# Kernel tuning notes

Hardware: AMD Instinct MI355X
Metric: run time of the kernel (lower is better)

## Reference

```python
import jax, jax.numpy as jnp
import numpy as np

B, S, V, H, L, NH, DH, F = 1, 512, 30522, 768, 12, 12, 64, 3072
N, E, GH, NC = 50000, 800000, 128, 3


def setup_inputs() -> dict:
    key = jax.random.key(0)
    ks = iter(jax.random.split(key, 48))
    def nrm(shape, s=0.02):
        return jax.random.normal(next(ks), shape, jnp.float32) * s
    inp = {
        "input_ids": jax.random.randint(next(ks), (B, S), 0, V, dtype=jnp.int32),
        "attention_mask": jnp.ones((B, S), jnp.int32),
        "token_type_ids": jnp.zeros((B, S), jnp.int32),
        "premise_edge_index": jax.random.randint(next(ks), (2, E), 0, N, dtype=jnp.int32),
        "hypothesis_edge_index": jax.random.randint(next(ks), (2, E), 0, N, dtype=jnp.int32),
        "premise_node_features": nrm((N, H), 1.0),
        "hypothesis_node_features": nrm((N, H), 1.0),
        "word_emb": nrm((V, H)), "pos_emb": nrm((S, H)), "type_emb": nrm((2, H)),
        "emb_ln_s": jnp.ones((H,)), "emb_ln_b": jnp.zeros((H,)),
        "Wq": nrm((L, H, H)), "bq": jnp.zeros((L, H)),
        "Wk": nrm((L, H, H)), "bk": jnp.zeros((L, H)),
        "Wv": nrm((L, H, H)), "bv": jnp.zeros((L, H)),
        "Wo": nrm((L, H, H)), "bo": jnp.zeros((L, H)),
        "ln1_s": jnp.ones((L, H)), "ln1_b": jnp.zeros((L, H)),
        "W1": nrm((L, H, F)), "b1": jnp.zeros((L, F)),
        "W2": nrm((L, F, H)), "b2": jnp.zeros((L, H)),
        "ln2_s": jnp.ones((L, H)), "ln2_b": jnp.zeros((L, H)),
        "gcn_W1": nrm((H, GH), 0.05), "gcn_b1": jnp.zeros((GH,)),
        "gcn_W2": nrm((GH, GH), 0.05), "gcn_b2": jnp.zeros((GH,)),
        "comb_W": nrm((2 * (H + GH), H)), "comb_b": jnp.zeros((H,)),
        "cls_W": nrm((H, NC)), "cls_b": jnp.zeros((NC,)),
    }
    return inp


def _ln(x, s, b, eps=1e-12):
    m = jnp.mean(x, -1, keepdims=True)
    v = jnp.mean(jnp.square(x - m), -1, keepdims=True)
    return (x - m) * jax.lax.rsqrt(v + eps) * s + b


def _gcn(x, edge_index, W1, b1, W2, b2):
    # PyG GCNConv: add self-loops, symmetric D^-1/2 A D^-1/2 normalization,
    # linear transform first, then scatter-add messages at destination.
    n = x.shape[0]
    loops = jnp.arange(n, dtype=edge_index.dtype)
    src = jnp.concatenate([edge_index[0], loops])
    dst = jnp.concatenate([edge_index[1], loops])
    deg = jax.ops.segment_sum(jnp.ones(src.shape[0], jnp.float32), dst, num_segments=n)
    dinv = jnp.where(deg > 0, jax.lax.rsqrt(jnp.maximum(deg, 1e-12)), 0.0)
    norm = (dinv[src] * dinv[dst])[:, None]
    def conv(h, W, b):
        hw = h @ W
        return jax.ops.segment_sum(hw[src] * norm, dst, num_segments=n) + b
    h = jax.nn.relu(conv(x, W1, b1))
    h = conv(h, W2, b2)
    # global_mean_pool with batch=None -> single graph mean, shape [1, GH]
    return jnp.mean(h, axis=0, keepdims=True)


def _bert(input_ids, attention_mask, token_type_ids, word_emb, pos_emb, type_emb, emb_ln_s, emb_ln_b, layer_params):
    s = input_ids.shape[1]
    h = word_emb[input_ids] + pos_emb[None, :s] + type_emb[token_type_ids]
    h = _ln(h, emb_ln_s, emb_ln_b)
    bias = (1.0 - attention_mask.astype(jnp.float32))[:, None, None, :] * -1e4
    def step(h, p):
        wq, bq, wk, bk, wv, bv, wo, bo, l1s, l1b, w1, b1_, w2, b2_, l2s, l2b = p
        b_, s_, _ = h.shape
        q = (h @ wq + bq).reshape(b_, s_, NH, DH)
        k = (h @ wk + bk).reshape(b_, s_, NH, DH)
        v = (h @ wv + bv).reshape(b_, s_, NH, DH)
        scores = jnp.einsum('bqhd,bkhd->bhqk', q, k) / np.float32(np.sqrt(DH)) + bias
        ctx = jnp.einsum('bhqk,bkhd->bqhd', jax.nn.softmax(scores, -1), v).reshape(b_, s_, H)
        h1 = _ln(h + ctx @ wo + bo, l1s, l1b)
        f = jax.nn.gelu(h1 @ w1 + b1_, approximate=False) @ w2 + b2_
        return _ln(h1 + f, l2s, l2b), None
    h, _ = jax.lax.scan(step, h, layer_params)
    return h[:, 0, :]  # CLS pooling, [B, H]


def reference(input_ids, attention_mask, token_type_ids, premise_edge_index, premise_node_features, hypothesis_edge_index, hypothesis_node_features, word_emb, pos_emb, type_emb, emb_ln_s, emb_ln_b, Wq, bq, Wk, bk, Wv, bv, Wo, bo, ln1_s, ln1_b, W1, b1, W2, b2, ln2_s, ln2_b, gcn_W1, gcn_b1, gcn_W2, gcn_b2, comb_W, comb_b, cls_W, cls_b):
    lp = (Wq, bq, Wk, bk, Wv, bv, Wo, bo, ln1_s, ln1_b, W1, b1, W2, b2, ln2_s, ln2_b)
    cls = _bert(input_ids, attention_mask, token_type_ids, word_emb, pos_emb, type_emb, emb_ln_s, emb_ln_b, lp)
    gp = _gcn(premise_node_features, premise_edge_index, gcn_W1, gcn_b1, gcn_W2, gcn_b2)
    gh = _gcn(hypothesis_node_features, hypothesis_edge_index, gcn_W1, gcn_b1, gcn_W2, gcn_b2)
    cp = jnp.concatenate([cls, gp], -1)
    ch = jnp.concatenate([cls, gh], -1)
    fc = jnp.concatenate([cp, ch], -1)  # [1, 2*(H+GH)]
    feat = jax.nn.relu(fc @ comb_W + comb_b)  # dropout is identity at eval
    return feat @ cls_W + cls_b
```

## Files before the change

### kernel.cpp

```cpp
#include <hip/hip_runtime.h>
#include <math.h>

constexpr int kS = 512, kH = 768, kNH = 12, kDH = 64, kF = 3072, kL = 12;
constexpr int kN = 50000, kE = 800000, kGH = 128;

#define CDIV(a,b) (((a)+(b)-1)/(b))

struct Ptr3 { const float* p[3]; };

typedef __attribute__((ext_vector_type(8))) short bf16x8;
typedef __attribute__((ext_vector_type(4))) float f32x4;

__device__ __forceinline__ unsigned short bf16_rne(float f) {
    unsigned int u = __float_as_uint(f);
    u += 0x7fffu + ((u >> 16) & 1u);
    return (unsigned short)(u >> 16);
}
__device__ __forceinline__ float bf16_f32(unsigned short h) {
    return __uint_as_float(((unsigned int)h) << 16);
}
__device__ __forceinline__ void split2(float f, short& hi, short& lo) {
    unsigned short h = bf16_rne(f);
    hi = (short)h;
    lo = (short)bf16_rne(f - bf16_f32(h));
}

constexpr int LDR = 72;

__global__ void fill_kernel(float* p, float v, long n) {
    long i = blockIdx.x * (long)blockDim.x + threadIdx.x;
    if (i < n) p[i] = v;
}

__global__ void gcn_zero_kernel(int* icnt, float* wsum, float* svec) {
    int i = blockIdx.x * 256 + threadIdx.x;
    if (i < kN) { icnt[i] = 0; wsum[i] = 0.f; }
    if (i < kGH) svec[i] = 0.f;
}

__global__ void embed_ln_kernel(const int* ids, const int* tt, const int* mask,
                                const float* we, const float* pe, const float* te,
                                const float* g, const float* b, float* out,
                                short* oh, short* ol, float* mb) {
    int s = blockIdx.x;
    int tid = threadIdx.x;
    __shared__ float red[256];
    if (tid == 0) mb[s] = (1.f - (float)mask[s]) * -1e4f;
    int id = ids[s], t = tt[s];
    float vals[3]; float sum = 0.f;
    #pragma unroll
    for (int r = 0; r < 3; r++) {
        int j = tid + r * 256;
        float x = we[(long)id * kH + j] + pe[(long)s * kH + j] + te[(long)t * kH + j];
        vals[r] = x; sum += x;
    }
    red[tid] = sum; __syncthreads();
    for (int off = 128; off > 0; off >>= 1) { if (tid < off) red[tid] += red[tid + off]; __syncthreads(); }
    float mean = red[0] / kH; __syncthreads();
    float vs = 0.f;
    #pragma unroll
    for (int r = 0; r < 3; r++) { float d = vals[r] - mean; vs += d * d; }
    red[tid] = vs; __syncthreads();
    for (int off = 128; off > 0; off >>= 1) { if (tid < off) red[tid] += red[tid + off]; __syncthreads(); }
    float rstd = rsqrtf(red[0] / kH + 1e-12f);
    #pragma unroll
    for (int r = 0; r < 3; r++) {
        int j = tid + r * 256;
        float o = (vals[r] - mean) * rstd * g[j] + b[j];
        out[(long)s * kH + j] = o;
        short hi, lo; split2(o, hi, lo);
        oh[(long)s * kH + j] = hi; ol[(long)s * kH + j] = lo;
    }
}

__global__ void wtrans_all_kernel(const float* __restrict__ W, short* __restrict__ Th,
                                  short* __restrict__ Tl, int K, int N, long ostride) {
    int z = blockIdx.z;
    const float* Wm = W + (long)z * K * N;
    long moff = (long)z * ostride;
    __shared__ short th[32][33], tl[32][33];
    int n0 = blockIdx.x * 32, k0 = blockIdx.y * 32;
    int c = threadIdx.x & 31, r = threadIdx.x >> 5;
    #pragma unroll
    for (int p = 0; p < 4; p++) {
        int rr = p * 8 + r;
        float f = Wm[(long)(k0 + rr) * N + n0 + c];
        short hi, lo; split2(f, hi, lo);
        th[rr][c] = hi; tl[rr][c] = lo;
    }
    __syncthreads();
    #pragma unroll
    for (int p = 0; p < 4; p++) {
        int rr = p * 8 + r;
        Th[moff + (long)(n0 + rr) * K + k0 + c] = th[c][rr];
        Tl[moff + (long)(n0 + rr) * K + k0 + c] = tl[c][rr];
    }
}

__global__ void vtrans_kernel(const short* __restrict__ vh, const short* __restrict__ vl,
                              short* __restrict__ vth, short* __restrict__ vtl) {
    __shared__ short th[32][33], tl[32][33];
    int s0 = blockIdx.x * 32;
    int h = blockIdx.y >> 1, d0 = (blockIdx.y & 1) * 32;
    int c = threadIdx.x & 31, r = threadIdx.x >> 5;
    #pragma unroll
    for (int p = 0; p < 4; p++) {
        int rr = p * 8 + r;
        th[rr][c] = vh[(long)(s0 + rr) * kH + h * kDH + d0 + c];
        tl[rr][c] = vl[(long)(s0 + rr) * kH + h * kDH + d0 + c];
    }
    __syncthreads();
    #pragma unroll
    for (int p = 0; p < 4; p++) {
        int rr = p * 8 + r;
        vth[((long)h * kDH + d0 + rr) * kS + s0 + c] = th[c][rr];
        vtl[((long)h * kDH + d0 + rr) * kS + s0 + c] = tl[c][rr];
    }
}

__global__ __launch_bounds__(256, 4) void gemm64_pre(
    const short* __restrict__ Ah, const short* __restrict__ Al,
    const short* __restrict__ Bth, const short* __restrict__ Btl, long wstride,
    float* __restrict__ part, int M, int Nn, int K, int S)
{
    __shared__ short As[64 * LDR], Bs[128 * LDR];
    int w = blockIdx.z / S, s = blockIdx.z % S;
    const short* Bh_ = Bth + (long)w * wstride;
    const short* Bl_ = Btl + (long)w * wstride;
    int Kc = K / S, kbeg = s * Kc;
    int m0 = blockIdx.y * 64, n0 = blockIdx.x * 128;
    int tid = threadIdx.x;
    int ar = tid >> 2, aq = (tid & 3) * 8;
    const short* Agh = Ah + (long)(m0 + ar) * K + kbeg + aq;
    const short* Agl = Al + (long)(m0 + ar) * K + kbeg + aq;
    int aofs = ar * LDR + aq;
    int br = tid >> 1, bq = (tid & 1) * 16;
    const short* Bgh = Bh_ + (long)(n0 + br) * K + kbeg + bq;
    const short* Bgl = Bl_ + (long)(n0 + br) * K + kbeg + bq;
    int bofs = br * LDR + bq;
    int wid = tid >> 6, lane = tid & 63;
    int wm = (wid >> 1) * 32, wn = (wid & 1) * 64;
    int fr = lane & 15, ko = (lane >> 4) * 8;
    f32x4 acc[2][4];
    #pragma unroll
    for (int i = 0; i < 2; i++)
        #pragma unroll
        for (int j = 0; j < 4; j++) acc[i][j] = (f32x4){0.f, 0.f, 0.f, 0.f};
    int nst = Kc / 32;
    bf16x8 pa0 = *(const bf16x8*)(Agh);
    bf16x8 pa1 = *(const bf16x8*)(Agl);
    bf16x8 pb0 = *(const bf16x8*)(Bgh);
    bf16x8 pb1 = *(const bf16x8*)(Bgh + 8);
    bf16x8 pb2 = *(const bf16x8*)(Bgl);
    bf16x8 pb3 = *(const bf16x8*)(Bgl + 8);
    for (int st = 0; st < nst; ++st) {
        *(bf16x8*)&As[aofs]      = pa0;
        *(bf16x8*)&As[aofs + 32] = pa1;
        *(bf16x8*)&Bs[bofs]      = pb0;
        *(bf16x8*)&Bs[bofs + 8]  = pb1;
        *(bf16x8*)&Bs[bofs + 32] = pb2;
        *(bf16x8*)&Bs[bofs + 40] = pb3;
        if (st + 1 < nst) {
            int go = (st + 1) * 32;
            pa0 = *(const bf16x8*)(Agh + go);
            pa1 = *(const bf16x8*)(Agl + go);
            pb0 = *(const bf16x8*)(Bgh + go);
            pb1 = *(const bf16x8*)(Bgh + go + 8);
            pb2 = *(const bf16x8*)(Bgl + go);
            pb3 = *(const bf16x8*)(Bgl + go + 8);
        }
        __syncthreads();
        bf16x8 bh[4], bl[4];
        #pragma unroll
        for (int j = 0; j < 4; j++) {
            int c = (wn + j * 16 + fr) * LDR + ko;
            bh[j] = *(const bf16x8*)&Bs[c];
            bl[j] = *(const bf16x8*)&Bs[c + 32];
        }
        #pragma unroll
        for (int i = 0; i < 2; i++) {
            int r = (wm + i * 16 + fr) * LDR + ko;
            bf16x8 ah = *(const bf16x8*)&As[r];
            bf16x8 al = *(const bf16x8*)&As[r + 32];
            #pragma unroll
            for (int j = 0; j < 4; j++) {
                acc[i][j] = __builtin_amdgcn_mfma_f32_16x16x32_bf16(ah, bh[j], acc[i][j], 0, 0, 0);
                acc[i][j] = __builtin_amdgcn_mfma_f32_16x16x32_bf16(ah, bl[j], acc[i][j], 0, 0, 0);
                acc[i][j] = __builtin_amdgcn_mfma_f32_16x16x32_bf16(al, bh[j], acc[i][j], 0, 0, 0);
            }
        }
        __syncthreads();
    }
    long MN = (long)M * Nn;
    float* Pp = part + (long)(w * S + s) * MN;
    int cr = (lane >> 4) * 4;
    #pragma unroll
    for (int i = 0; i < 2; i++) {
        #pragma unroll
        for (int r = 0; r < 4; r++) {
            int gm = m0 + wm + i * 16 + cr + r;
            float* rowp = &Pp[(long)gm * Nn + n0 + wn + fr];
            #pragma unroll
            for (int j = 0; j < 4; j++) rowp[j * 16] = acc[i][j][r];
        }
    }
}

__global__ __launch_bounds__(256, 4) void gemm64_gcn(
    const float* __restrict__ A,
    const short* __restrict__ Bth, const short* __restrict__ Btl,
    float* __restrict__ part, int M, int Nn, int K, int S)
{
    __shared__ short As[64 * LDR], Bs[128 * LDR];
    int s = blockIdx.z;
    int Kc = K / S, kbeg = s * Kc;
    int m0 = blockIdx.y * 64, n0 = blockIdx.x * 128;
    int tid = threadIdx.x;
    int ar = tid >> 2, aqf = (tid & 3) * 8;
    int gmA = m0 + ar; if (gmA > M - 1) gmA = M - 1;
    const float* Agf = A + (long)gmA * K + kbeg + aqf;
    int aofs = ar * LDR + aqf;
    int br = tid >> 1, bq = (tid & 1) * 16;
    const short* Bgh = Bth + (long)(n0 + br) * K + kbeg + bq;
    const short* Bgl = Btl + (long)(n0 + br) * K + kbeg + bq;
    int bofs = br * LDR + bq;
    int wid = tid >> 6, lane = tid & 63;
    int wm = (wid >> 1) * 32, wn = (wid & 1) * 64;
    int fr = lane & 15, ko = (lane >> 4) * 8;
    f32x4 acc[2][4];
    #pragma unroll
    for (int i = 0; i < 2; i++)
        #pragma unroll
        for (int j = 0; j < 4; j++) acc[i][j] = (f32x4){0.f, 0.f, 0.f, 0.f};
    int nst = Kc / 32;
    float4 pf0 = *(const float4*)(Agf);
    float4 pf1 = *(const float4*)(Agf + 4);
    bf16x8 pb0 = *(const bf16x8*)(Bgh);
    bf16x8 pb1 = *(const bf16x8*)(Bgh + 8);
    bf16x8 pb2 = *(const bf16x8*)(Bgl);
    bf16x8 pb3 = *(const bf16x8*)(Bgl + 8);
    for (int st = 0; st < nst; ++st) {
        short h0, l0, h1, l1, h2, l2, h3, l3, h4, l4, h5, l5, h6, l6, h7, l7;
        split2(pf0.x, h0, l0); split2(pf0.y, h1, l1); split2(pf0.z, h2, l2); split2(pf0.w, h3, l3);
        split2(pf1.x, h4, l4); split2(pf1.y, h5, l5); split2(pf1.z, h6, l6); split2(pf1.w, h7, l7);
        *(short4*)&As[aofs]      = make_short4(h0, h1, h2, h3);
        *(short4*)&As[aofs + 4]  = make_short4(h4, h5, h6, h7);
        *(short4*)&As[aofs + 32] = make_short4(l0, l1, l2, l3);
        *(short4*)&As[aofs + 36] = make_short4(l4, l5, l6, l7);
        *(bf16x8*)&Bs[bofs]      = pb0;
        *(bf16x8*)&Bs[bofs + 8]  = pb1;
        *(bf16x8*)&Bs[bofs + 32] = pb2;
        *(bf16x8*)&Bs[bofs + 40] = pb3;
        if (st + 1 < nst) {
            int go = (st + 1) * 32;
            pf0 = *(const float4*)(Agf + go);
            pf1 = *(const float4*)(Agf + go + 4);
            pb0 = *(const bf16x8*)(Bgh + go);
            pb1 = *(const bf16x8*)(Bgh + go + 8);
            pb2 = *(const bf16x8*)(Bgl + go);
            pb3 = *(const bf16x8*)(Bgl + go + 8);
        }
        __syncthreads();
        bf16x8 bh[4], bl[4];
        #pragma unroll
        for (int j = 0; j < 4; j++) {
            int c = (wn + j * 16 + fr) * LDR + ko;
            bh[j] = *(const bf16x8*)&Bs[c];
            bl[j] = *(const bf16x8*)&Bs[c + 32];
        }
        #pragma unroll
        for (int i = 0; i < 2; i++) {
            int r = (wm + i * 16 + fr) * LDR + ko;
            bf16x8 ah = *(const bf16x8*)&As[r];
            bf16x8 al = *(const bf16x8*)&As[r + 32];
            #pragma unroll
            for (int j = 0; j < 4; j++) {
                acc[i][j] = __builtin_amdgcn_mfma_f32_16x16x32_bf16(ah, bh[j], acc[i][j], 0, 0, 0);
                acc[i][j] = __builtin_amdgcn_mfma_f32_16x16x32_bf16(ah, bl[j], acc[i][j], 0, 0, 0);
                acc[i][j] = __builtin_amdgcn_mfma_f32_16x16x32_bf16(al, bh[j], acc[i][j], 0, 0, 0);
            }
        }
        __syncthreads();
    }
    long MN = (long)M * Nn;
    float* Pp = part + (long)s * MN;
    int cr = (lane >> 4) * 4;
    #pragma unroll
    for (int i = 0; i < 2; i++) {
        #pragma unroll
        for (int r = 0; r < 4; r++) {
            int gm = m0 + wm + i * 16 + cr + r;
            if (gm >= M) continue;
            float* rowp = &Pp[(long)gm * Nn + n0 + wn + fr];
            #pragma unroll
            for (int j = 0; j < 4; j++) rowp[j * 16] = acc[i][j][r];
        }
    }
}

__global__ __launch_bounds__(128) void flash_attn_kernel(
    const short* __restrict__ qh, const short* __restrict__ ql,
    const short* __restrict__ kh, const short* __restrict__ kl,
    const short* __restrict__ vth, const short* __restrict__ vtl,
    const float* __restrict__ mb,
    short* __restrict__ ctxh, short* __restrict__ ctxl)
{
    __shared__ short Qs[2 * 64 * LDR];
    __shared__ short Ks[128 * LDR];
    __shared__ short Ps[4 * 64 * 40];
    int h = blockIdx.y;
    int q0 = blockIdx.x * 64;
    int tid = threadIdx.x;
    int wid = tid >> 6, lane = tid & 63;
    int wm = wid * 32;
    int fr = lane & 15, ko = (lane >> 4) * 8;
    int cr4 = (lane >> 4) * 4;
    {
        int row = tid >> 1, dseg = tid & 1;
        const short* gh_ = qh + (long)(q0 + row) * kH + h * kDH + dseg * 32;
        const short* gl_ = ql + (long)(q0 + row) * kH + h * kDH + dseg * 32;
        short* dst = &Qs[(dseg * 64 + row) * LDR];
        #pragma unroll
        for (int c = 0; c < 4; c++) {
            *(bf16x8*)&dst[c * 8]      = *(const bf16x8*)(gh_ + c * 8);
            *(bf16x8*)&dst[32 + c * 8] = *(const bf16x8*)(gl_ + c * 8);
        }
    }
    float mrun[2][4], lrun[2][4];
    f32x4 accO[2][4];
    #pragma unroll
    for (int i = 0; i < 2; i++)
        #pragma unroll
        for (int r = 0; r < 4; r++) { mrun[i][r] = -1e30f; lrun[i][r] = 0.f; }
    #pragma unroll
    for (int i = 0; i < 2; i++)
        #pragma unroll
        for (int j = 0; j < 4; j++) accO[i][j] = (f32x4){0.f, 0.f, 0.f, 0.f};

    for (int t = 0; t < 4; ++t) {
        int k0t = t * 128;
        f32x4 accS[2][8];
        #pragma unroll
        for (int i = 0; i < 2; i++)
            #pragma unroll
            for (int j = 0; j < 8; j++) accS[i][j] = (f32x4){0.f, 0.f, 0.f, 0.f};
        for (int st = 0; st < 2; ++st) {
            __syncthreads();
            {
                int row = tid;
                const short* gh_ = kh + (long)(k0t + row) * kH + h * kDH + st * 32;
                const short* gl_ = kl + (long)(k0t + row) * kH + h * kDH + st * 32;
                short* dst = &Ks[row * LDR];
                #pragma unroll
                for (int c = 0; c < 4; c++) {
                    *(bf16x8*)&dst[c * 8]      = *(const bf16x8*)(gh_ + c * 8);
                    *(bf16x8*)&dst[32 + c * 8] = *(const bf16x8*)(gl_ + c * 8);
                }
            }
            __syncthreads();
            bf16x8 bh[8], bl[8];
            #pragma unroll
            for (int j = 0; j < 8; j++) {
                int c = (j * 16 + fr) * LDR + ko;
                bh[j] = *(const bf16x8*)&Ks[c];
                bl[j] = *(const bf16x8*)&Ks[c + 32];
            }
            #pragma unroll
            for (int i = 0; i < 2; i++) {
                int r = (st * 64 + wm + i * 16 + fr) * LDR + ko;
                bf16x8 ah = *(const bf16x8*)&Qs[r];
                bf16x8 al = *(const bf16x8*)&Qs[r + 32];
                #pragma unroll
                for (int j = 0; j < 8; j++) {
                    accS[i][j] = __builtin_amdgcn_mfma_f32_16x16x32_bf16(ah, bh[j], accS[i][j], 0, 0, 0);
                    accS[i][j] = __builtin_amdgcn_mfma_f32_16x16x32_bf16(ah, bl[j], accS[i][j], 0, 0, 0);
                    accS[i][j] = __builtin_amdgcn_mfma_f32_16x16x32_bf16(al, bh[j], accS[i][j], 0, 0, 0);
                }
            }
        }
        float mbv[8];
        #pragma unroll
        for (int j = 0; j < 8; j++) mbv[j] = mb[k0t + j * 16 + fr];
        #pragma unroll
        for (int i = 0; i < 2; i++) {
            #pragma unroll
            for (int r = 0; r < 4; r++) {
                float mt = -1e30f;
                #pragma unroll
                for (int j = 0; j < 8; j++) {
                    float sv = accS[i][j][r] * 0.125f + mbv[j];
                    accS[i][j][r] = sv;
                    mt = fmaxf(mt, sv);
                }
                #pragma unroll
                for (int mmask = 1; mmask < 16; mmask <<= 1)
                    mt = fmaxf(mt, __shfl_xor(mt, mmask, 64));
                float mn = fmaxf(mrun[i][r], mt);
                float sc = __expf(mrun[i][r] - mn);
                mrun[i][r] = mn;
                lrun[i][r] *= sc;
                #pragma unroll
                for (int jo = 0; jo < 4; jo++) {
                    accO[i][jo][r] *= sc;
                }
                float lt = 0.f;
                #pragma unroll
                for (int j = 0; j < 8; j++) {
                    float p = __expf(accS[i][j][r] - mn);
                    accS[i][j][r] = p;
                    lt += p;
                }
                #pragma unroll
                for (int mmask = 1; mmask < 16; mmask <<= 1)
                    lt += __shfl_xor(lt, mmask, 64);
                lrun[i][r] += lt;
            }
        }
        #pragma unroll
        for (int i = 0; i < 2; i++)
            #pragma unroll
            for (int j = 0; j < 8; j++)
                #pragma unroll
                for (int r = 0; r < 4; r++) {
                    int rowp = wm + i * 16 + cr4 + r;
                    Ps[(j >> 1) * 2560 + rowp * 40 + (j & 1) * 16 + fr] =
                        (short)bf16_rne(accS[i][j][r]);
                }
        for (int st2 = 0; st2 < 4; ++st2) {
            __syncthreads();
            {
                int row = tid >> 1, half = tid & 1;
                const short* gh_ = vth + ((long)h * kDH + row) * kS + k0t + st2 * 32 + half * 16;
                const short* gl_ = vtl + ((long)h * kDH + row) * kS + k0t + st2 * 32 + half * 16;
                short* dst = &Ks[row * LDR + half * 16];
                *(bf16x8*)&dst[0]  = *(const bf16x8*)(gh_);
                *(bf16x8*)&dst[8]  = *(const bf16x8*)(gh_ + 8);
                *(bf16x8*)&dst[32] = *(const bf16x8*)(gl_);
                *(bf16x8*)&dst[40] = *(const bf16x8*)(gl_ + 8);
            }
            __syncthreads();
            bf16x8 vh_[4], vl_[4];
            #pragma unroll
            for (int j = 0; j < 4; j++) {
                int c = (j * 16 + fr) * LDR + ko;
                vh_[j] = *(const bf16x8*)&Ks[c];
                vl_[j] = *(const bf16x8*)&Ks[c + 32];
            }
            #pragma unroll
            for (int i = 0; i < 2; i++) {
                bf16x8 pa = *(const bf16x8*)&Ps[st2 * 2560 + (wm + i * 16 + fr) * 40 + ko];
                #pragma unroll
                for (int j = 0; j < 4; j++) {
                    accO[i][j] = __builtin_amdgcn_mfma_f32_16x16x32_bf16(pa, vh_[j], accO[i][j], 0, 0, 0);
                    accO[i][j] = __builtin_amdgcn_mfma_f32_16x16x32_bf16(pa, vl_[j], accO[i][j], 0, 0, 0);
                }
            }
        }
        __syncthreads();
        #pragma unroll
        for (int i = 0; i < 2; i++)
            #pragma unroll
            for (int j = 0; j < 8; j++)
                #pragma unroll
                for (int r = 0; r < 4; r++) {
                    int rowp = wm + i * 16 + cr4 + r;
                    float p = accS[i][j][r];
                    unsigned short ph = bf16_rne(p);
                    Ps[(j >> 1) * 2560 + rowp * 40 + (j & 1) * 16 + fr] =
                        (short)bf16_rne(p - bf16_f32(ph));
                }
        for (int st2 = 0; st2 < 4; ++st2) {
            __syncthreads();
            {
                int row = tid >> 1, half = tid & 1;
                const short* gh_ = vth + ((long)h * kDH + row) * kS + k0t + st2 * 32 + half * 16;
                short* dst = &Ks[row * LDR + half * 16];
                *(bf16x8*)&dst[0] = *(const bf16x8*)(gh_);
                *(bf16x8*)&dst[8] = *(const bf16x8*)(gh_ + 8);
            }
            __syncthreads();
            bf16x8 vh_[4];
            #pragma unroll
            for (int j = 0; j < 4; j++)
                vh_[j] = *(const bf16x8*)&Ks[(j * 16 + fr) * LDR + ko];
            #pragma unroll
            for (int i = 0; i < 2; i++) {
                bf16x8 pa = *(const bf16x8*)&Ps[st2 * 2560 + (wm + i * 16 + fr) * 40 + ko];
                #pragma unroll
                for (int j = 0; j < 4; j++)
                    accO[i][j] = __builtin_amdgcn_mfma_f32_16x16x32_bf16(pa, vh_[j], accO[i][j], 0, 0, 0);
            }
        }
        __syncthreads();
    }
    #pragma unroll
    for (int i = 0; i < 2; i++) {
        #pragma unroll
        for (int r = 0; r < 4; r++) {
            float inv = 1.f / lrun[i][r];
            int q = q0 + wm + i * 16 + cr4 + r;
            #pragma unroll
            for (int j = 0; j < 4; j++) {
                float o = accO[i][j][r] * inv;
                int col = h * kDH + j * 16 + fr;
                short hi, lo; split2(o, hi, lo);
                ctxh[(long)q * kH + col] = hi;
                ctxl[(long)q * kH + col] = lo;
            }
        }
    }
}

__global__ void splitk_epi_qkv_kernel(const float* __restrict__ part, Ptr3 bias,
                                      short* __restrict__ qh, short* __restrict__ ql,
                                      short* __restrict__ kh, short* __restrict__ kl,
                                      short* __restrict__ vh, short* __restrict__ vl,
                                      int S) {
    const long MN = (long)kS * kH;
    int w = blockIdx.y;
    long i = ((long)blockIdx.x * blockDim.x + threadIdx.x) * 4;
    if (i >= MN) return;
    const float* P = part + (long)w * S * MN + i;
    float4 a = *(const float4*)P;
    for (int s2 = 1; s2 < S; ++s2) {
        float4 b2 = *(const float4*)(P + (long)s2 * MN);
        a.x += b2.x; a.y += b2.y; a.z += b2.z; a.w += b2.w;
    }
    const float* bw = bias.p[w];
    int n = (int)(i % kH);
    a.x += bw[n]; a.y += bw[n + 1]; a.z += bw[n + 2]; a.w += bw[n + 3];
    short* oh = (w == 0) ? qh : (w == 1) ? kh : vh;
    short* ol = (w == 0) ? ql : (w == 1) ? kl : vl;
    short h0, l0, h1, l1, h2, l2, h3, l3;
    split2(a.x, h0, l0); split2(a.y, h1, l1); split2(a.z, h2, l2); split2(a.w, h3, l3);
    *(short4*)&oh[i] = make_short4(h0, h1, h2, h3);
    *(short4*)&ol[i] = make_short4(l0, l1, l2, l3);
}

__global__ void splitk_epi_sh_kernel(const float* __restrict__ part, const float* __restrict__ bias,
                                     short* __restrict__ oh, short* __restrict__ ol,
                                     long MN, int Nn, int S, int act) {
    long i = ((long)blockIdx.x * blockDim.x + threadIdx.x) * 4;
    if (i >= MN) return;
    const float* P = part + i;
    float4 a = *(const float4*)P;
    for (int s2 = 1; s2 < S; ++s2) {
        float4 b2 = *(const float4*)(P + (long)s2 * MN);
        a.x += b2.x; a.y += b2.y; a.z += b2.z; a.w += b2.w;
    }
    if (bias) {
        int n = (int)(i % Nn);
        a.x += bias[n]; a.y += bias[n + 1]; a.z += bias[n + 2]; a.w += bias[n + 3];
    }
    if (act == 1) {
        a.x = 0.5f * a.x * (1.f + erff(a.x * 0.70710678118654752f));
        a.y = 0.5f * a.y * (1.f + erff(a.y * 0.70710678118654752f));
        a.z = 0.5f * a.z * (1.f + erff(a.z * 0.70710678118654752f));
        a.w = 0.5f * a.w * (1.f + erff(a.w * 0.70710678118654752f));
    }
    short h0, l0, h1, l1, h2, l2, h3, l3;
    split2(a.x, h0, l0); split2(a.y, h1, l1); split2(a.z, h2, l2); split2(a.w, h3, l3);
    *(short4*)&oh[i] = make_short4(h0, h1, h2, h3);
    *(short4*)&ol[i] = make_short4(l0, l1, l2, l3);
}

__global__ void splitk_epi_ln2_kernel(const float* __restrict__ part, const float* __restrict__ bias,
                                      const float* __restrict__ res, const float* __restrict__ g,
                                      const float* __restrict__ b, float* __restrict__ out,
                                      short* __restrict__ oh, short* __restrict__ ol, int S) {
    int row = blockIdx.x; int tid = threadIdx.x;
    __shared__ float red[256];
    const long MN = (long)kS * kH;
    float vals[3]; float sum = 0.f;
    #pragma unroll
    for (int r = 0; r < 3; r++) {
        int j = tid + r * 256;
        const float* P = part + (long)row * kH + j;
        float x = res[(long)row * kH + j] + bias[j];
        for (int s2 = 0; s2 < S; ++s2) x += P[(long)s2 * MN];
        vals[r] = x; sum += x;
    }
    red[tid] = sum; __syncthreads();
    for (int off = 128; off > 0; off >>= 1) { if (tid < off) red[tid] += red[tid + off]; __syncthreads(); }
    float mean = red[0] / kH; __syncthreads();
    float vs = 0.f;
    #pragma unroll
    for (int r = 0; r < 3; r++) { float d = vals[r] - mean; vs += d * d; }
    red[tid] = vs; __syncthreads();
    for (int off = 128; off > 0; off >>= 1) { if (tid < off) red[tid] += red[tid + off]; __syncthreads(); }
    float rstd = rsqrtf(red[0] / kH + 1e-12f);
    #pragma unroll
    for (int r = 0; r < 3; r++) {
        int j = tid + r * 256;
        float o = (vals[r] - mean) * rstd * g[j] + b[j];
        out[(long)row * kH + j] = o;
        short hi, lo; split2(o, hi, lo);
        oh[(long)row * kH + j] = hi; ol[(long)row * kH + j] = lo;
    }
}

__global__ void cnt_kernel(const int* __restrict__ dst, int* __restrict__ cnt, int E) {
    int e = blockIdx.x * blockDim.x + threadIdx.x;
    if (e < E) atomicAdd(&cnt[dst[e]], 1);
}

__global__ void scan1_kernel(const int* __restrict__ cnt, int* __restrict__ offs,
                             int* __restrict__ bsum, int n) {
    __shared__ int sh[256];
    int i = blockIdx.x * 256 + threadIdx.x;
    int v = (i < n) ? cnt[i] : 0;
    sh[threadIdx.x] = v; __syncthreads();
    for (int off = 1; off < 256; off <<= 1) {
        int t = (threadIdx.x >= off) ? sh[threadIdx.x - off] : 0;
        __syncthreads();
        sh[threadIdx.x] += t;
        __syncthreads();
    }
    if (i < n) offs[i] = sh[threadIdx.x] - v;
    if (threadIdx.x == 255) bsum[blockIdx.x] = sh[255];
}

__global__ void scan2_kernel(int* bsum, int nb, int* offs, int n) {
    if (threadIdx.x == 0) {
        int run = 0;
        for (int b = 0; b < nb; b++) { int t = bsum[b]; bsum[b] = run; run += t; }
        offs[n] = run;
    }
}

__global__ void scan3_kernel(const int* __restrict__ cnt, int* __restrict__ offs,
                             const int* __restrict__ bsum, int* __restrict__ cur,
                             float* __restrict__ dinv, int n) {
    int i = blockIdx.x * 256 + threadIdx.x;
    if (i >= n) return;
    int o = offs[i] + bsum[blockIdx.x];
    offs[i] = o; cur[i] = o;
    dinv[i] = rsqrtf((float)(cnt[i] + 1));
}

__global__ void csrfill_edgew_kernel(const int* __restrict__ src, const int* __restrict__ dst,
                                     int* __restrict__ cur, int* __restrict__ csr,
                                     const float* __restrict__ dinv, float* __restrict__ wsum,
                                     int E) {
    int e = blockIdx.x * blockDim.x + threadIdx.x;
    if (e < E) {
        int s2 = src[e], d = dst[e];
        int slot = atomicAdd(&cur[d], 1);
        csr[slot] = s2;
        atomicAdd(&wsum[s2], dinv[s2] * dinv[d]);
    }
}

__global__ __launch_bounds__(256) void spmm_gather_kernel(const int* __restrict__ offs,
                                                          const int* __restrict__ csr,
                                                          const float* __restrict__ dinv,
                                                          const float* __restrict__ hw,
                                                          const float* __restrict__ b1,
                                                          float* __restrict__ hout, int n) {
    int d = blockIdx.x * 2 + (threadIdx.x >> 7);
    int j = threadIdx.x & 127;
    if (d >= n) return;
    int beg = offs[d], end = offs[d + 1];
    float a0 = 0.f, a1 = 0.f, a2 = 0.f, a3 = 0.f;
    float a4 = 0.f, a5 = 0.f, a6 = 0.f, a7 = 0.f;
    int p = beg;
    for (; p + 8 <= end; p += 8) {
        int s0 = csr[p], s1 = csr[p + 1], s2 = csr[p + 2], s3 = csr[p + 3];
        int s4 = csr[p + 4], s5 = csr[p + 5], s6 = csr[p + 6], s7 = csr[p + 7];
        a0 += dinv[s0] * hw[(long)s0 * kGH + j];
        a1 += dinv[s1] * hw[(long)s1 * kGH + j];
        a2 += dinv[s2] * hw[(long)s2 * kGH + j];
        a3 += dinv[s3] * hw[(long)s3 * kGH + j];
        a4 += dinv[s4] * hw[(long)s4 * kGH + j];
        a5 += dinv[s5] * hw[(long)s5 * kGH + j];
        a6 += dinv[s6] * hw[(long)s6 * kGH + j];
        a7 += dinv[s7] * hw[(long)s7 * kGH + j];
    }
    for (; p < end; ++p) {
        int s8 = csr[p];
        a0 += dinv[s8] * hw[(long)s8 * kGH + j];
    }
    float acc = ((a0 + a1) + (a2 + a3)) + ((a4 + a5) + (a6 + a7));
    float dd = dinv[d];
    float v = acc * dd + dd * dd * hw[(long)d * kGH + j] + b1[j];
    hout[(long)d * kGH + j] = fmaxf(v, 0.f);
}

__global__ void wreduce_kernel(const float* __restrict__ h, const float* __restrict__ w,
                               const float* __restrict__ dinv, float* __restrict__ s, int n) {
    int tid = threadIdx.x; int j = tid & 127; int half = tid >> 7;
    float acc = 0.f;
    for (int u = blockIdx.x * 2 + half; u < n; u += gridDim.x * 2) {
        float di = dinv[u];
        acc += (w[u] + di * di) * h[(long)u * kGH + j];
    }
    __shared__ float red[256];
    red[tid] = acc; __syncthreads();
    if (tid < 128) atomicAdd(&s[j], red[tid] + red[tid + 128]);
}

__global__ void gcn_final_kernel(const float* s, const float* W2, const float* b2, float* g) {
    int j2 = threadIdx.x;
    float acc = 0.f;
    for (int j = 0; j < kGH; j++) acc += s[j] * W2[(long)j * kGH + j2];
    g[j2] = acc * (1.f / (float)kN) + b2[j2];
}

__global__ void combine_part_kernel(const float* __restrict__ cls, const float* __restrict__ gp,
                                    const float* __restrict__ gh, const float* __restrict__ Wc,
                                    float* __restrict__ feat) {
    int i0 = blockIdx.x * 32;
    int tid = threadIdx.x;
    float a0 = 0.f, a1 = 0.f, a2 = 0.f;
    for (int r = 0; r < 32; r++) {
        int i = i0 + r;
        float x = (i < 768) ? cls[i] : (i < 896) ? gp[i - 768]
                : (i < 1664) ? cls[i - 896] : gh[i - 1664];
        const float* row = Wc + (long)i * kH;
        a0 += x * row[tid]; a1 += x * row[tid + 256]; a2 += x * row[tid + 512];
    }
    atomicAdd(&feat[tid], a0);
    atomicAdd(&feat[tid + 256], a1);
    atomicAdd(&feat[tid + 512], a2);
}

__global__ void combine_fin_kernel(float* feat, const float* bc) {
    int o = blockIdx.x * 256 + threadIdx.x;
    if (o < kH) feat[o] = fmaxf(feat[o] + bc[o], 0.f);
}

__global__ void cls_head_kernel(const float* feat, const float* W, const float* b, float* out) {
    int tid = threadIdx.x;
    float a0 = 0.f, a1 = 0.f, a2 = 0.f;
    for (int o = tid; o < kH; o += 256) {
        float f = feat[o];
        a0 += f * W[o * 3 + 0]; a1 += f * W[o * 3 + 1]; a2 += f * W[o * 3 + 2];
    }
    __shared__ float r0[256], r1[256], r2[256];
    r0[tid] = a0; r1[tid] = a1; r2[tid] = a2; __syncthreads();
    for (int off = 128; off > 0; off >>= 1) {
        if (tid < off) { r0[tid] += r0[tid + off]; r1[tid] += r1[tid + off]; r2[tid] += r2[tid + off]; }
        __syncthreads();
    }
    if (tid == 0) { out[0] = r0[0] + b[0]; out[1] = r1[0] + b[1]; out[2] = r2[0] + b[2]; }
}

extern "C" void kernel_launch(void* const* d_in, const int* in_sizes, int n_in,
                              void* d_out, int out_size, void* d_ws, size_t ws_size,
                              hipStream_t stream) {
    const int*   input_ids = (const int*)d_in[0];
    const int*   attn_mask = (const int*)d_in[1];
    const int*   type_ids  = (const int*)d_in[2];
    const int*   p_edges   = (const int*)d_in[3];
    const int*   h_edges   = (const int*)d_in[4];
    const float* p_nodes   = (const float*)d_in[5];
    const float* h_nodes   = (const float*)d_in[6];
    const float* word_emb  = (const float*)d_in[7];
    const float* pos_emb   = (const float*)d_in[8];
    const float* type_emb  = (const float*)d_in[9];
    const float* eln_s     = (const float*)d_in[10];
    const float* eln_b     = (const float*)d_in[11];
    const float* Wq = (const float*)d_in[12]; const float* bq = (const float*)d_in[13];
    const float* Wk = (const float*)d_in[14]; const float* bk = (const float*)d_in[15];
    const float* Wv = (const float*)d_in[16]; const float* bv = (const float*)d_in[17];
    const float* Wo = (const float*)d_in[18]; const float* bo = (const float*)d_in[19];
    const float* l1s = (const float*)d_in[20]; const float* l1b = (const float*)d_in[21];
    const float* W1 = (const float*)d_in[22]; const float* b1 = (const float*)d_in[23];
    const float* W2 = (const float*)d_in[24]; const float* b2 = (const float*)d_in[25];
    const float* l2s = (const float*)d_in[26]; const float* l2b = (const float*)d_in[27];
    const float* gW1 = (const float*)d_in[28]; const float* gb1 = (const float*)d_in[29];
    const float* gW2 = (const float*)d_in[30]; const float* gb2 = (const float*)d_in[31];
    const float* cW  = (const float*)d_in[32]; const float* cb  = (const float*)d_in[33];
    const float* clsW = (const float*)d_in[34]; const float* clsB = (const float*)d_in[35];
    float* out = (float*)d_out;

    float* W = (float*)d_ws;
    size_t off = 0;
    auto alloc = [&](size_t n) { float* p = W + off; off += n; return p; };
    float* h    = alloc((size_t)kS * kH);
    float* h1   = alloc((size_t)kS * kH);
    float* deg  = alloc(kN);
    float* wsum = alloc(kN);
    float* svec = alloc(kGH);
    float* gp   = alloc(kGH);
    float* ghv  = alloc(kGH);
    float* mb   = alloc(kS);
    float* feat = alloc(kH);
    float* big  = W + off;

    float* part  = big;
    short* ffn1_h = (short*)(big + 7864320);
    short* ffn1_l = ffn1_h + (size_t)1572864;
    short* sm    = (short*)(big + 11796480);
    const size_t SMN = (size_t)kS * kH;
    short* q_h = sm;            short* q_l = q_h + SMN;
    short* k_h = q_l + SMN;     short* k_l = k_h + SMN;
    short* v_h = k_l + SMN;     short* v_l = v_h + SMN;
    short* vt_h = v_l + SMN;    short* vt_l = vt_h + SMN;
    short* ctx_h = vt_l + SMN;  short* ctx_l = ctx_h + SMN;
    short* h1_h = ctx_l + SMN;  short* h1_l = h1_h + SMN;
    short* hh_h = h1_l + SMN;   short* hh_l = hh_h + SMN;

    float* hw1 = big;
    float* agg = big + (size_t)kN * kGH;
    int* icnt  = (int*)(big + 2 * (size_t)kN * kGH);
    int* ioffs = icnt + 50048;
    int* icur  = ioffs + 50048;
    int* ibsum = icur + 50048;
    int* icsr  = ibsum + 256;
    short* gwt_h = (short*)(icsr + kE);
    short* gwt_l = gwt_h + (size_t)kH * kGH;

    const size_t QKV_SZ = (size_t)kH * kH;
    const size_t FF_SZ  = (size_t)kH * kF;
    short* wc = (short*)(big + 15000000);
    short* qkv_h = wc;                          short* qkv_l = qkv_h + 12 * 3 * QKV_SZ;
    short* wo_h  = qkv_l + 12 * 3 * QKV_SZ;     short* wo_l  = wo_h + 12 * QKV_SZ;
    short* w1_h  = wo_l + 12 * QKV_SZ;          short* w1_l  = w1_h + 12 * FF_SZ;
    short* w2_h  = w1_l + 12 * FF_SZ;           short* w2_l  = w2_h + 12 * FF_SZ;

    const long MN_H = (long)kS * kH;
    const long MN_F = (long)kS * kF;
    const int nScanBlk = CDIV(kN, 256);

    wtrans_all_kernel<<<dim3(24, 24, 12), 256, 0, stream>>>(Wq, qkv_h,              qkv_l,              kH, kH, (long)(3 * QKV_SZ));
    wtrans_all_kernel<<<dim3(24, 24, 12), 256, 0, stream>>>(Wk, qkv_h + QKV_SZ,     qkv_l + QKV_SZ,     kH, kH, (long)(3 * QKV_SZ));
    wtrans_all_kernel<<<dim3(24, 24, 12), 256, 0, stream>>>(Wv, qkv_h + 2 * QKV_SZ, qkv_l + 2 * QKV_SZ, kH, kH, (long)(3 * QKV_SZ));
    wtrans_all_kernel<<<dim3(24, 24, 12), 256, 0, stream>>>(Wo, wo_h, wo_l, kH, kH, (long)QKV_SZ);
    wtrans_all_kernel<<<dim3(96, 24, 12), 256, 0, stream>>>(W1, w1_h, w1_l, kH, kF, (long)FF_SZ);
    wtrans_all_kernel<<<dim3(24, 96, 12), 256, 0, stream>>>(W2, w2_h, w2_l, kF, kH, (long)FF_SZ);

    const int* gsrc[2] = { p_edges, h_edges };
    const int* gdst[2] = { p_edges + kE, h_edges + kE };
    const float* gx[2] = { p_nodes, h_nodes };
    float* gout[2] = { gp, ghv };
    wtrans_all_kernel<<<dim3(kGH / 32, kH / 32, 1), 256, 0, stream>>>(gW1, gwt_h, gwt_l, kH, kGH, 0);
    for (int gi = 0; gi < 2; gi++) {
        gcn_zero_kernel<<<nScanBlk, 256, 0, stream>>>(icnt, wsum, svec);
        cnt_kernel<<<CDIV(kE, 256), 256, 0, stream>>>(gdst[gi], icnt, kE);
        scan1_kernel<<<nScanBlk, 256, 0, stream>>>(icnt, ioffs, ibsum, kN);
        scan2_kernel<<<1, 64, 0, stream>>>(ibsum, nScanBlk, ioffs, kN);
        scan3_kernel<<<nScanBlk, 256, 0, stream>>>(icnt, ioffs, ibsum, icur, deg, kN);
        csrfill_edgew_kernel<<<CDIV(kE, 256), 256, 0, stream>>>(
            gsrc[gi], gdst[gi], icur, icsr, deg, wsum, kE);
        gemm64_gcn<<<dim3(1, CDIV(kN, 64), 1), 256, 0, stream>>>(
            gx[gi], gwt_h, gwt_l, hw1, kN, kGH, kH, 1);
        spmm_gather_kernel<<<CDIV(kN, 2), 256, 0, stream>>>(ioffs, icsr, deg, hw1, gb1, agg, kN);
        wreduce_kernel<<<512, 256, 0, stream>>>(agg, wsum, deg, svec, kN);
        gcn_final_kernel<<<1, kGH, 0, stream>>>(svec, gW2, gb2, gout[gi]);
    }

    embed_ln_kernel<<<kS, 256, 0, stream>>>(input_ids, type_ids, attn_mask,
                                            word_emb, pos_emb, type_emb,
                                            eln_s, eln_b, h, hh_h, hh_l, mb);
    for (int l = 0; l < kL; l++) {
        const float* bq_l = bq + (size_t)l * kH;
        const float* bk_l = bk + (size_t)l * kH;
        const float* bv_l = bv + (size_t)l * kH;
        const float* bo_l = bo + (size_t)l * kH;
        const float* b1_l = b1 + (size_t)l * kF;
        const float* b2_l = b2 + (size_t)l * kH;
        const float* l1s_l = l1s + (size_t)l * kH; const float* l1b_l = l1b + (size_t)l * kH;
        const float* l2s_l = l2s + (size_t)l * kH; const float* l2b_l = l2b + (size_t)l * kH;
        const short* qkvh_l = qkv_h + (size_t)l * 3 * QKV_SZ;
        const short* qkvl_l = qkv_l + (size_t)l * 3 * QKV_SZ;
        const short* woh_l = wo_h + (size_t)l * QKV_SZ;
        const short* wol_l = wo_l + (size_t)l * QKV_SZ;
        const short* w1h_l = w1_h + (size_t)l * FF_SZ;
        const short* w1l_l = w1_l + (size_t)l * FF_SZ;
        const short* w2h_l = w2_h + (size_t)l * FF_SZ;
        const short* w2l_l = w2_l + (size_t)l * FF_SZ;

        gemm64_pre<<<dim3(kH / 128, kS / 64, 12), 256, 0, stream>>>(
            hh_h, hh_l, qkvh_l, qkvl_l, (long)QKV_SZ, part, kS, kH, kH, 4);
        splitk_epi_qkv_kernel<<<dim3((int)(MN_H / 4 / 256), 3), 256, 0, stream>>>(
            part, Ptr3{{bq_l, bk_l, bv_l}}, q_h, q_l, k_h, k_l, v_h, v_l, 4);
        vtrans_kernel<<<dim3(kS / 32, kNH * 2), 256, 0, stream>>>(v_h, v_l, vt_h, vt_l);
        flash_attn_kernel<<<dim3(kS / 64, kNH), 128, 0, stream>>>(
            q_h, q_l, k_h, k_l, vt_h, vt_l, mb, ctx_h, ctx_l);
        gemm64_pre<<<dim3(kH / 128, kS / 64, 8), 256, 0, stream>>>(
            ctx_h, ctx_l, woh_l, wol_l, 0, part, kS, kH, kH, 8);
        splitk_epi_ln2_kernel<<<kS, 256, 0, stream>>>(part, bo_l, h, l1s_l, l1b_l, h1, h1_h, h1_l, 8);
        gemm64_pre<<<dim3(kF / 128, kS / 64, 4), 256, 0, stream>>>(
            h1_h, h1_l, w1h_l, w1l_l, 0, part, kS, kF, kH, 4);
        splitk_epi_sh_kernel<<<(int)(MN_F / 4 / 256), 256, 0, stream>>>(
            part, b1_l, ffn1_h, ffn1_l, MN_F, kF, 4, 1);
        gemm64_pre<<<dim3(kH / 128, kS / 64, 8), 256, 0, stream>>>(
            ffn1_h, ffn1_l, w2h_l, w2l_l, 0, part, kS, kH, kF, 8);
        splitk_epi_ln2_kernel<<<kS, 256, 0, stream>>>(part, b2_l, h1, l2s_l, l2b_l, h, hh_h, hh_l, 8);
    }

    fill_kernel<<<3, 256, 0, stream>>>(feat, 0.f, kH);
    combine_part_kernel<<<56, 256, 0, stream>>>(h, gp, ghv, cW, feat);
    combine_fin_kernel<<<3, 256, 0, stream>>>(feat, cb);
    cls_head_kernel<<<1, 256, 0, stream>>>(feat, clsW, clsB, out);
}
```

Before: 2.418 ms.

## Fuse attention P·V passes, raise QKV split-k, fold small tail kernels

Flash attention now stores the hi and lo bf16 parts of P in separate shared buffers. It computes all three split-precision products in one pass over the V tiles instead of a second pass that reloads V. The QKV GEMM split-k factor goes from 4 to 6 for more parallelism. The feat zeroing moves into the embedding kernel and the bias+ReLU into the classifier head, removing two launches. The costs are more shared memory, which may lower occupancy, and a larger split-k partial buffer, which may exceed its allocation.

```diff
diff --git a/kernel.cpp b/kernel.cpp
--- a/kernel.cpp
+++ b/kernel.cpp
@@ -41,11 +41,12 @@
 __global__ void embed_ln_kernel(const int* ids, const int* tt, const int* mask,
                                 const float* we, const float* pe, const float* te,
                                 const float* g, const float* b, float* out,
-                                short* oh, short* ol, float* mb) {
+                                short* oh, short* ol, float* mb, float* feat) {
     int s = blockIdx.x;
     int tid = threadIdx.x;
     __shared__ float red[256];
     if (tid == 0) mb[s] = (1.f - (float)mask[s]) * -1e4f;
+    if (s == 0) { feat[tid] = 0.f; feat[tid + 256] = 0.f; feat[tid + 512] = 0.f; }
     int id = ids[s], t = tt[s];
     float vals[3]; float sum = 0.f;
     #pragma unroll
@@ -307,7 +308,8 @@
 {
     __shared__ short Qs[2 * 64 * LDR];
     __shared__ short Ks[128 * LDR];
-    __shared__ short Ps[4 * 64 * 40];
+    __shared__ short Psh[4 * 64 * 40];
+    __shared__ short Psl[4 * 64 * 40];
     int h = blockIdx.y;
     int q0 = blockIdx.x * 64;
     int tid = threadIdx.x;
@@ -400,9 +402,7 @@
                 mrun[i][r] = mn;
                 lrun[i][r] *= sc;
                 #pragma unroll
-                for (int jo = 0; jo < 4; jo++) {
-                    accO[i][jo][r] *= sc;
-                }
+                for (int jo = 0; jo < 4; jo++) accO[i][jo][r] *= sc;
                 float lt = 0.f;
                 #pragma unroll
                 for (int j = 0; j < 8; j++) {
@@ -423,8 +423,11 @@
                 #pragma unroll
                 for (int r = 0; r < 4; r++) {
                     int rowp = wm + i * 16 + cr4 + r;
-                    Ps[(j >> 1) * 2560 + rowp * 40 + (j & 1) * 16 + fr] =
-                        (short)bf16_rne(accS[i][j][r]);
+                    int idx = (j >> 1) * 2560 + rowp * 40 + (j & 1) * 16 + fr;
+                    float p = accS[i][j][r];
+                    unsigned short ph = bf16_rne(p);
+                    Psh[idx] = (short)ph;
+                    Psl[idx] = (short)bf16_rne(p - bf16_f32(ph));
                 }
         for (int st2 = 0; st2 < 4; ++st2) {
             __syncthreads();
@@ -448,47 +451,15 @@
             }
             #pragma unroll
             for (int i = 0; i < 2; i++) {
-                bf16x8 pa = *(const bf16x8*)&Ps[st2 * 2560 + (wm + i * 16 + fr) * 40 + ko];
+                int pidx = st2 * 2560 + (wm + i * 16 + fr) * 40 + ko;
+                bf16x8 pah = *(const bf16x8*)&Psh[pidx];
+                bf16x8 pal = *(const bf16x8*)&Psl[pidx];
                 #pragma unroll
                 for (int j = 0; j < 4; j++) {
-                    accO[i][j] = __builtin_amdgcn_mfma_f32_16x16x32_bf16(pa, vh_[j], accO[i][j], 0, 0, 0);
-                    accO[i][j] = __builtin_amdgcn_mfma_f32_16x16x32_bf16(pa, vl_[j], accO[i][j], 0, 0, 0);
+                    accO[i][j] = __builtin_amdgcn_mfma_f32_16x16x32_bf16(pah, vh_[j], accO[i][j], 0, 0, 0);
+                    accO[i][j] = __builtin_amdgcn_mfma_f32_16x16x32_bf16(pah, vl_[j], accO[i][j], 0, 0, 0);
+                    accO[i][j] = __builtin_amdgcn_mfma_f32_16x16x32_bf16(pal, vh_[j], accO[i][j], 0, 0, 0);
                 }
-            }
-        }
-        __syncthreads();
-        #pragma unroll
-        for (int i = 0; i < 2; i++)
-            #pragma unroll
-            for (int j = 0; j < 8; j++)
-                #pragma unroll
-                for (int r = 0; r < 4; r++) {
-                    int rowp = wm + i * 16 + cr4 + r;
-                    float p = accS[i][j][r];
-                    unsigned short ph = bf16_rne(p);
-                    Ps[(j >> 1) * 2560 + rowp * 40 + (j & 1) * 16 + fr] =
-                        (short)bf16_rne(p - bf16_f32(ph));
-                }
-        for (int st2 = 0; st2 < 4; ++st2) {
-            __syncthreads();
-            {
-                int row = tid >> 1, half = tid & 1;
-                const short* gh_ = vth + ((long)h * kDH + row) * kS + k0t + st2 * 32 + half * 16;
-                short* dst = &Ks[row * LDR + half * 16];
-                *(bf16x8*)&dst[0] = *(const bf16x8*)(gh_);
-                *(bf16x8*)&dst[8] = *(const bf16x8*)(gh_ + 8);
-            }
-            __syncthreads();
-            bf16x8 vh_[4];
-            #pragma unroll
-            for (int j = 0; j < 4; j++)
-                vh_[j] = *(const bf16x8*)&Ks[(j * 16 + fr) * LDR + ko];
-            #pragma unroll
-            for (int i = 0; i < 2; i++) {
-                bf16x8 pa = *(const bf16x8*)&Ps[st2 * 2560 + (wm + i * 16 + fr) * 40 + ko];
-                #pragma unroll
-                for (int j = 0; j < 4; j++)
-                    accO[i][j] = __builtin_amdgcn_mfma_f32_16x16x32_bf16(pa, vh_[j], accO[i][j], 0, 0, 0);
             }
         }
         __syncthreads();
@@ -724,16 +695,12 @@
     atomicAdd(&feat[tid + 512], a2);
 }
 
-__global__ void combine_fin_kernel(float* feat, const float* bc) {
-    int o = blockIdx.x * 256 + threadIdx.x;
-    if (o < kH) feat[o] = fmaxf(feat[o] + bc[o], 0.f);
-}
-
-__global__ void cls_head_kernel(const float* feat, const float* W, const float* b, float* out) {
+__global__ void cls_head_kernel(const float* feat, const float* bc,
+                                const float* W, const float* b, float* out) {
     int tid = threadIdx.x;
     float a0 = 0.f, a1 = 0.f, a2 = 0.f;
     for (int o = tid; o < kH; o += 256) {
-        float f = feat[o];
+        float f = fmaxf(feat[o] + bc[o], 0.f);
         a0 += f * W[o * 3 + 0]; a1 += f * W[o * 3 + 1]; a2 += f * W[o * 3 + 2];
     }
     __shared__ float r0[256], r1[256], r2[256];
@@ -852,7 +819,7 @@
 
     embed_ln_kernel<<<kS, 256, 0, stream>>>(input_ids, type_ids, attn_mask,
                                             word_emb, pos_emb, type_emb,
-                                            eln_s, eln_b, h, hh_h, hh_l, mb);
+                                            eln_s, eln_b, h, hh_h, hh_l, mb, feat);
     for (int l = 0; l < kL; l++) {
         const float* bq_l = bq + (size_t)l * kH;
         const float* bk_l = bk + (size_t)l * kH;
@@ -871,10 +838,10 @@
         const short* w2h_l = w2_h + (size_t)l * FF_SZ;
         const short* w2l_l = w2_l + (size_t)l * FF_SZ;
 
-        gemm64_pre<<<dim3(kH / 128, kS / 64, 12), 256, 0, stream>>>(
-            hh_h, hh_l, qkvh_l, qkvl_l, (long)QKV_SZ, part, kS, kH, kH, 4);
+        gemm64_pre<<<dim3(kH / 128, kS / 64, 18), 256, 0, stream>>>(
+            hh_h, hh_l, qkvh_l, qkvl_l, (long)QKV_SZ, part, kS, kH, kH, 6);
         splitk_epi_qkv_kernel<<<dim3((int)(MN_H / 4 / 256), 3), 256, 0, stream>>>(
-            part, Ptr3{{bq_l, bk_l, bv_l}}, q_h, q_l, k_h, k_l, v_h, v_l, 4);
+            part, Ptr3{{bq_l, bk_l, bv_l}}, q_h, q_l, k_h, k_l, v_h, v_l, 6);
         vtrans_kernel<<<dim3(kS / 32, kNH * 2), 256, 0, stream>>>(v_h, v_l, vt_h, vt_l);
         flash_attn_kernel<<<dim3(kS / 64, kNH), 128, 0, stream>>>(
             q_h, q_l, k_h, k_l, vt_h, vt_l, mb, ctx_h, ctx_l);
@@ -890,8 +857,6 @@
         splitk_epi_ln2_kernel<<<kS, 256, 0, stream>>>(part, b2_l, h1, l2s_l, l2b_l, h, hh_h, hh_l, 8);
     }
 
-    fill_kernel<<<3, 256, 0, stream>>>(feat, 0.f, kH);
     combine_part_kernel<<<56, 256, 0, stream>>>(h, gp, ghv, cW, feat);
-    combine_fin_kernel<<<3, 256, 0, stream>>>(feat, cb);
-    cls_head_kernel<<<1, 256, 0, stream>>>(feat, clsW, clsB, out);
-}
+    cls_head_kernel<<<1, 256, 0, stream>>>(feat, cb, clsW, clsB, out);
+}
```

Result: no change. 2.445 ms (+1.1%).
